# Kernel optimization log

Measured on AMD Instinct MI355X. Metric: run time of the kernel, lower is better.

The kernel has to match this reference:

```python
import jax, jax.numpy as jnp
import numpy as np

CLP_K = 9
SCL_KS = (3, 4, 3)  # scl0_k, scl1_k, scl2_k from the source


def _ste(f, x):
    # straight-through estimator: forward f(x), identity gradient
    return x + jax.lax.stop_gradient(f(x) - x)


def floor_ste(x):
    return _ste(jnp.floor, x)


def round_ste(x):
    return _ste(jnp.round, x)


def conv_t(x, w, b):
    # torch F.conv_transpose2d with kernel 5, stride 2, padding 2, output_padding 1
    # expressed as an lhs-dilated conv; w is torch layout [in, out, kh, kw]
    k = w.shape[-1]
    wc = jnp.flip(w, axis=(-2, -1)).transpose(1, 0, 2, 3)  # -> [out, in, kh, kw]
    lo = k - 1 - 2           # k-1-padding = 2
    hi = k - 1 - 2 + 1       # + output_padding = 3
    y = jax.lax.conv_general_dilated(
        x, wc, window_strides=(1, 1), padding=[(lo, hi), (lo, hi)],
        lhs_dilation=(2, 2), dimension_numbers=('NCHW', 'OIHW', 'NCHW'))
    return y + b[None, :, None, None]


def split_deconv(x, w, b, split):
    # sum of `split` transposed convs with floor((round(W)+j)/split) quantized weights
    out = 0.0
    for j in range(split):
        wj = floor_ste((round_ste(w) + j) / split)
        bj = floor_ste((round_ste(b) + j) / split)
        out = out + conv_t(x, wj, bj)
    return out


def _g_s_forward(x, ws, bs, ms, relus, dv, Bits, split):
    # clp[i] = round((2^Bits - 1) / relus[i] * 2^(16+clp_k))
    clp = jnp.round((2.0 ** Bits - 1.0) / relus * 2.0 ** (16 + CLP_K))
    for i in range(3):
        x = split_deconv(x, ws[i], bs[i], split)
        x = x * ms[i][None, :, None, None]
        x = floor_ste((x + 2.0 ** (dv[i] - 1 - CLP_K)) / 2.0 ** (dv[i] - CLP_K))
        x = jnp.clip(x, 0.0, clp[i])
        sk = SCL_KS[i]
        scl = floor_ste((relus[i] + 2.0 ** (sk - 1)) / 2.0 ** sk)
        x = floor_ste((x * scl + 2.0 ** (15 + CLP_K - sk)) / 2.0 ** (16 + CLP_K - sk))
    x = split_deconv(x, ws[3], bs[3], split)
    x = x * ms[3][None, :, None, None]
    x = floor_ste((x + 2.0 ** (dv[3] - 9)) / 2.0 ** (dv[3] - 8))
    return x / 255.0


def setup_inputs() -> dict:
    key = jax.random.key(0)
    ks = jax.random.split(key, 16)
    N, M = 192, 320
    B, h, w = 1, 48, 48
    x = jax.random.randint(ks[0], (B, M, h, w), 0, 256).astype(jnp.float32)
    w1 = jax.random.normal(ks[1], (M, N, 5, 5), jnp.float32) * 20.0
    b1 = jax.random.normal(ks[2], (N,), jnp.float32) * 20.0
    w2 = jax.random.normal(ks[3], (N, N, 5, 5), jnp.float32) * 20.0
    b2 = jax.random.normal(ks[4], (N,), jnp.float32) * 20.0
    w3 = jax.random.normal(ks[5], (N, N, 5, 5), jnp.float32) * 20.0
    b3 = jax.random.normal(ks[6], (N,), jnp.float32) * 20.0
    w4 = jax.random.normal(ks[7], (N, 3, 5, 5), jnp.float32) * 20.0
    b4 = jax.random.normal(ks[8], (3,), jnp.float32) * 20.0
    muls0 = jax.random.randint(ks[9], (N,), 1, 1000).astype(jnp.float32)
    muls1 = jax.random.randint(ks[10], (N,), 1, 1000).astype(jnp.float32)
    muls2 = jax.random.randint(ks[11], (N,), 1, 1000).astype(jnp.float32)
    muls3 = jax.random.randint(ks[12], (3,), 1, 1000).astype(jnp.float32)
    relus = jnp.array([40000.0, 36000.0, 30000.0], jnp.float32)
    muls_dvds = jnp.array([24, 24, 24, 24], jnp.int32)
    return {"x": x, "w1": w1, "b1": b1, "w2": w2, "b2": b2, "w3": w3,
            "b3": b3, "w4": w4, "b4": b4, "muls0": muls0, "muls1": muls1,
            "muls2": muls2, "muls3": muls3, "relus": relus,
            "muls_dvds": muls_dvds, "Bits": 8, "split": 4}


def reference(x, w1, b1, w2, b2, w3, b3, w4, b4,
              muls0, muls1, muls2, muls3, relus, muls_dvds, Bits, split):
    dv = muls_dvds.astype(jnp.float32)
    ws = (w1, w2, w3, w4)
    bs = (b1, b2, b3, b4)
    ms = (muls0, muls1, muls2, muls3)
    return _g_s_forward(x, ws, bs, ms, relus, dv, int(Bits), int(split))
```

## Files before the change

kernel.cpp:

```cpp
#include <hip/hip_runtime.h>
#include <cmath>


typedef int int4v  __attribute__((ext_vector_type(4)));
typedef int int16v __attribute__((ext_vector_type(16)));

__device__ __forceinline__ void tap_to_k(int t, int& ky, int& kx) {
    if (t < 9)       { int dy = t/3,  dx = t%3;                   ky = 4-2*dy; kx = 4-2*dx; }
    else if (t < 15) { int u = t-9;   int dy = u/2, dx = 1+(u&1);  ky = 4-2*dy; kx = 5-2*dx; }
    else if (t < 21) { int u = t-15;  int dy = 1+u/3, dx = u%3;    ky = 5-2*dy; kx = 4-2*dx; }
    else             { int u = t-21;  int dy = 1+u/2, dx = 1+(u&1); ky = 5-2*dy; kx = 5-2*dx; }
}

__global__ __launch_bounds__(256)
void convert_x_t(const float* __restrict__ x, signed char* __restrict__ xh,
                 int C, int HW) {
    __shared__ float t[64][65];
    const int p0 = blockIdx.x * 64;
    const int c0 = blockIdx.y * 64;
    const int pL = threadIdx.x & 63;
    const int r0 = threadIdx.x >> 6;
    #pragma unroll
    for (int k = 0; k < 16; ++k) {
        int ciL = r0 * 16 + k;
        t[ciL][pL] = x[(size_t)(c0 + ciL) * HW + p0 + pL];
    }
    __syncthreads();
    #pragma unroll
    for (int k = 0; k < 16; ++k) {
        int pL2 = r0 * 16 + k;
        xh[(size_t)(p0 + pL2) * C + c0 + pL] = (signed char)((int)t[pL][pL2] - 128);
    }
}

__global__ __launch_bounds__(256)
void pack3(const float* __restrict__ w1, const float* __restrict__ w2,
           const float* __restrict__ w3,
           signed char* __restrict__ p1, signed char* __restrict__ p2,
           signed char* __restrict__ p3) {
    const int layer = blockIdx.y;
    const float* w = (layer == 0) ? w1 : (layer == 1) ? w2 : w3;
    signed char* out = (layer == 0) ? p1 : (layer == 1) ? p2 : p3;
    const int Cin = (layer == 0) ? 320 : 192;
    const int Cout = 192, NT = 6;
    int idx = blockIdx.x * 256 + threadIdx.x;
    if (idx >= Cin * Cout) return;
    const int co = idx % Cout, ci = idx / Cout;
    const float* wr = w + (size_t)(ci * Cout + co) * 25;
    float v[25];
    #pragma unroll
    for (int k = 0; k < 25; ++k) {
        float t = rintf(wr[k]);
        v[k] = fminf(fmaxf(t, -128.0f), 127.0f);
    }
    const int qs = ci >> 5, half = (ci >> 4) & 1, j = ci & 15;
    const int nb = co >> 5, lane = half * 32 + (co & 31);
    size_t base = ((size_t)(qs * NT + nb) * 25) * 1024 + lane * 16 + j;
    #pragma unroll
    for (int t = 0; t < 25; ++t) {
        int ky, kx; tap_to_k(t, ky, kx);
        out[base + (size_t)t * 1024] = (signed char)(int)v[ky * 5 + kx];
    }
}

__global__ void pack_w4_i8(const float* __restrict__ w, signed char* __restrict__ wpk) {
    int idx = blockIdx.x * blockDim.x + threadIdx.x;
    if (idx >= 6 * 9 * 64 * 16) return;
    int j    = idx & 15;
    int lane = (idx >> 4) & 63;
    int rem  = idx >> 10;
    int s9   = rem % 9;
    int qs   = rem / 9;
    int col  = lane & 31;
    int co   = col & 7;
    int p    = col >> 3;
    int py = p >> 1, px = p & 1;
    int dy = s9 / 3, dx = s9 % 3;
    int ci = qs * 32 + ((lane >> 5) << 4) + j;
    bool part = (py == 0 || dy >= 1) && (px == 0 || dx >= 1);
    float v = 0.0f;
    if (co < 3 && part) {
        int ky = py ? 5 - 2 * dy : 4 - 2 * dy;
        int kx = px ? 5 - 2 * dx : 4 - 2 * dx;
        v = rintf(w[(size_t)(ci * 3 + co) * 25 + ky * 5 + kx]);
        v = fminf(fmaxf(v, -128.0f), 127.0f);
    }
    wpk[idx] = (signed char)(int)v;
}

__global__ __launch_bounds__(64)
void tap4(const float* __restrict__ w1, const float* __restrict__ w2,
          const float* __restrict__ w3, const float* __restrict__ w4,
          int* __restrict__ t1, int* __restrict__ t2,
          int* __restrict__ t3, int* __restrict__ t4) {
    const int layer = blockIdx.y;
    const float* w = (layer == 0) ? w1 : (layer == 1) ? w2 : (layer == 2) ? w3 : w4;
    int* ts = (layer == 0) ? t1 : (layer == 1) ? t2 : (layer == 2) ? t3 : t4;
    const int Cin = (layer == 0) ? 320 : 192;
    const int Cout = (layer == 3) ? 3 : 192;
    const int i = blockIdx.x;
    if (i >= 4 * Cout) return;
    const int co = i % Cout, p = i / Cout;
    const int py = p >> 1, px = p & 1;
    const int nky = (5 - py + 1) >> 1;
    const int nkx = (5 - px + 1) >> 1;
    const int ntap = nky * nkx;
    int s = 0;
    for (int idx = threadIdx.x; idx < Cin * ntap; idx += 64) {
        const int ci = idx / ntap;
        const int u  = idx - ci * ntap;
        const int ky = py + 2 * (u / nkx);
        const int kx = px + 2 * (u % nkx);
        float v = rintf(w[(size_t)(ci * Cout + co) * 25 + ky * 5 + kx]);
        v = fminf(fmaxf(v, -128.0f), 127.0f);
        s += (int)v;
    }
    #pragma unroll
    for (int off = 32; off > 0; off >>= 1)
        s += __shfl_down(s, off, 64);
    if (threadIdx.x == 0) ts[i] = s;
}

__device__ __forceinline__ constexpr int role_nt(int role, int s9) {
    constexpr int NT0[9] = {1,1,1,1,2,2,1,2,2};
    constexpr int NT1[9] = {0,1,1,1,2,2,1,2,2};
    return role == 0 ? NT0[s9] : NT1[s9];
}
__device__ __forceinline__ constexpr int role_tap(int role, int s9, int u) {
    constexpr int T0[9][2] = {{0,0},{1,0},{2,0},{3,0},{4,21},{5,22},{6,0},{7,23},{8,24}};
    constexpr int T1[9][2] = {{0,0},{9,0},{10,0},{15,0},{11,16},{12,17},{18,0},{13,19},{14,20}};
    return role == 0 ? T0[s9][u] : T1[s9][u];
}
__device__ __forceinline__ constexpr int role_acc(int role, int s9, int u) {
    constexpr int A0[9][2] = {{0,0},{0,0},{0,0},{0,0},{0,1},{0,1},{0,0},{0,1},{0,1}};
    constexpr int A1[9][2] = {{0,0},{0,0},{0,0},{1,0},{0,1},{0,1},{1,0},{0,1},{0,1}};
    return role == 0 ? A0[s9][u] : A1[s9][u];
}

template<int ROLE, int R>
__device__ __forceinline__ void compute_role(const signed char* xs, const signed char* bs,
                                             int16v (&acc)[R][2], const int (&p0)[R],
                                             int half, int lane) {
    #pragma unroll
    for (int s9 = 0; s9 < 9; ++s9) {
        if (role_nt(ROLE, s9) == 0) continue;
        const int dy = s9 / 3, dx = s9 % 3;
        int4v a[R];
        #pragma unroll
        for (int r = 0; r < R; ++r)
            a[r] = *(const int4v*)&xs[(p0[r] + dy * 18 + dx) * 48 + half * 16];
        #pragma unroll
        for (int u = 0; u < 2; ++u) {
            if (u < role_nt(ROLE, s9)) {
                int4v b = *(const int4v*)&bs[role_tap(ROLE, s9, u) * 1024 + lane * 16];
                const int ai = role_acc(ROLE, s9, u);
                #pragma unroll
                for (int r = 0; r < R; ++r)
                    acc[r][ai] = __builtin_amdgcn_mfma_i32_32x32x32_i8(a[r], b, acc[r][ai], 0, 0, 0);
            }
        }
    }
}

template<int MW>
__global__ __launch_bounds__(MW * 64, 3)
void deconv_v7(const signed char* __restrict__ xin, const signed char* __restrict__ wpk,
               const float* __restrict__ bias, const float* __restrict__ muls,
               const int* __restrict__ tsum,
               const float* __restrict__ relus, const int* __restrict__ dvds,
               const int* __restrict__ bitsp,
               int layer, int Cin, int Cout, int NT, int Hq, int Wq,
               signed char* __restrict__ outp) {
    constexpr int R = 2;
    constexpr int PAIRS = MW / 2;
    constexpr int NROW = PAIRS * R * 2 + 2;
    constexpr int NPIX = NROW * 18;
    constexpr int THREADS = MW * 64;
    constexpr int XC = NPIX * 2;
    constexpr int XI = (XC + THREADS - 1) / THREADS;
    constexpr int BC = 1600;
    constexpr int BI = (BC + THREADS - 1) / THREADS;

    __shared__ __align__(16) signed char xs[NPIX * 48];
    __shared__ __align__(16) signed char bs[25600];

    const int tid  = threadIdx.x;
    const int lane = tid & 63;
    const int wid  = tid >> 6;
    const int pairId = wid >> 1;
    const int role   = wid & 1;
    const int qx0  = blockIdx.y * 16;
    const int qy0  = blockIdx.z * (PAIRS * R * 2);
    const int nb   = blockIdx.x;
    const int n0   = nb * 32;

    int16v acc[R][2];
    #pragma unroll
    for (int r = 0; r < R; ++r)
        #pragma unroll
        for (int p = 0; p < 2; ++p)
            #pragma unroll
            for (int e = 0; e < 16; ++e) acc[r][p][e] = 0;

    const int half   = lane >> 5;
    const int rowbit = (lane >> 4) & 1;
    const int col    = lane & 15;
    int p0[R];
    #pragma unroll
    for (int r = 0; r < R; ++r)
        p0[r] = ((pairId * R + r) * 2 + rowbit) * 18 + col;

    int4v xreg[XI], breg[BI];

    auto load_chunk = [&](int ck) {
        const signed char* wslab = wpk + (size_t)((ck >> 5) * NT + nb) * 25600;
        #pragma unroll
        for (int t = 0; t < XI; ++t) {
            int i = tid + t * THREADS;
            if (i < XC) {
                int pix = i >> 1, g = i & 1;
                int rr = pix / 18, cc = pix - rr * 18;
                int y = qy0 - 1 + rr, xx = qx0 - 1 + cc;
                int4v v = {(int)0x80808080, (int)0x80808080,
                           (int)0x80808080, (int)0x80808080};
                if ((unsigned)y < (unsigned)Hq && (unsigned)xx < (unsigned)Wq)
                    v = *(const int4v*)&xin[((size_t)y * Wq + xx) * Cin + ck + g * 16];
                xreg[t] = v;
            }
        }
        #pragma unroll
        for (int t = 0; t < BI; ++t) {
            int i = tid + t * THREADS;
            if (i < BC) breg[t] = *(const int4v*)&wslab[(size_t)i * 16];
        }
    };
    auto store_chunk = [&]() {
        #pragma unroll
        for (int t = 0; t < XI; ++t) {
            int i = tid + t * THREADS;
            if (i < XC) {
                int pix = i >> 1, g = i & 1;
                *(int4v*)&xs[pix * 48 + g * 16] = xreg[t];
            }
        }
        #pragma unroll
        for (int t = 0; t < BI; ++t) {
            int i = tid + t * THREADS;
            if (i < BC) *(int4v*)&bs[i * 16] = breg[t];
        }
    };

    load_chunk(0);
    for (int ck = 0; ck < Cin; ck += 32) {
        __syncthreads();
        store_chunk();
        __syncthreads();
        if (ck + 32 < Cin) load_chunk(ck + 32);

        if (role == 0) compute_role<0, R>(xs, bs, acc, p0, half, lane);
        else           compute_role<1, R>(xs, bs, acc, p0, half, lane);
    }

    const int dv = dvds[layer];
    float add1 = ldexpf(1.0f, dv - 10);
    float inv1 = ldexpf(1.0f, -(dv - 9));
    const float relu = relus[layer];
    const int sk = (layer == 1) ? 4 : 3;
    const float bitsv = ldexpf(1.0f, bitsp[0]) - 1.0f;
    float clp, scl;
    {
        #pragma clang fp contract(off)
        clp = rintf(bitsv / relu * 33554432.0f);
        scl = floorf((relu + ldexpf(1.0f, sk - 1)) * ldexpf(1.0f, -sk));
    }
    float add2 = ldexpf(1.0f, 24 - sk);
    float inv2 = ldexpf(1.0f, -(25 - sk));

    const int co = n0 + (lane & 31);
    float bq = rintf(bias[co]);
    float mm = muls[co];
    int pmap[2];
    pmap[0] = role == 0 ? 0 : 1;
    pmap[1] = role == 0 ? 3 : 2;
    int fullp[2];
    #pragma unroll
    for (int a = 0; a < 2; ++a) fullp[a] = tsum[pmap[a] * Cout + co];

    const int Wout = Wq * 2;

    #pragma unroll
    for (int r = 0; r < R; ++r) {
        #pragma unroll
        for (int a = 0; a < 2; ++a) {
            const int p = pmap[a];
            const int py = p >> 1, px = p & 1;
            #pragma unroll
            for (int reg = 0; reg < 16; ++reg) {
                const int mrow = (reg & 3) + 8 * (reg >> 2) + 4 * (lane >> 5);
                const int qy = qy0 + (pairId * R + r) * 2 + (mrow >> 4);
                const int qx = qx0 + (mrow & 15);
                float v = (float)(acc[r][a][reg] + 128 * fullp[a]);
                {
                    #pragma clang fp contract(off)
                    v = (v + bq) * mm;
                    v = floorf((v + add1) * inv1);
                    v = fminf(fmaxf(v, 0.0f), clp);
                    v = floorf((v * scl + add2) * inv2);
                }
                const int oy = 2 * qy + py, ox = 2 * qx + px;
                outp[((size_t)oy * Wout + ox) * Cout + co] = (signed char)((int)v - 128);
            }
        }
    }
}

__global__ __launch_bounds__(512, 3)
void deconv_final_v7(const signed char* __restrict__ xin, const signed char* __restrict__ wpk,
                     const float* __restrict__ bias, const float* __restrict__ muls,
                     const int* __restrict__ tsum, const int* __restrict__ dvds,
                     int Cin, int Hq, int Wq, float* __restrict__ outp) {
    constexpr int R = 2, MW = 8;
    constexpr int NROW = MW * R * 2 + 2;
    constexpr int NPIX = NROW * 18;
    constexpr int THREADS = 512;
    constexpr int XC = NPIX * 2;
    constexpr int XI = (XC + THREADS - 1) / THREADS;
    constexpr int BC = 576;
    constexpr int BI = (BC + THREADS - 1) / THREADS;

    __shared__ __align__(16) signed char xs[NPIX * 48];
    __shared__ __align__(16) signed char bs[9216];

    const int tid  = threadIdx.x;
    const int lane = tid & 63;
    const int wid  = tid >> 6;
    const int qx0  = blockIdx.y * 16;
    const int qy0  = blockIdx.z * (MW * R * 2);

    int16v acc[R];
    #pragma unroll
    for (int r = 0; r < R; ++r)
        #pragma unroll
        for (int e = 0; e < 16; ++e) acc[r][e] = 0;

    const int half   = lane >> 5;
    const int rowbit = (lane >> 4) & 1;
    const int col    = lane & 15;
    int p0[R];
    #pragma unroll
    for (int r = 0; r < R; ++r)
        p0[r] = ((wid * R + r) * 2 + rowbit) * 18 + col;

    int4v xreg[XI], breg[BI];

    auto load_chunk = [&](int ck) {
        const signed char* wslab = wpk + (size_t)(ck >> 5) * 9216;
        #pragma unroll
        for (int t = 0; t < XI; ++t) {
            int i = tid + t * THREADS;
            if (i < XC) {
                int pix = i >> 1, g = i & 1;
                int rr = pix / 18, cc = pix - rr * 18;
                int y = qy0 - 1 + rr, xx = qx0 - 1 + cc;
                int4v v = {(int)0x80808080, (int)0x80808080,
                           (int)0x80808080, (int)0x80808080};
                if ((unsigned)y < (unsigned)Hq && (unsigned)xx < (unsigned)Wq)
                    v = *(const int4v*)&xin[((size_t)y * Wq + xx) * Cin + ck + g * 16];
                xreg[t] = v;
            }
        }
        #pragma unroll
        for (int t = 0; t < BI; ++t) {
            int i = tid + t * THREADS;
            if (i < BC) breg[t] = *(const int4v*)&wslab[(size_t)i * 16];
        }
    };
    auto store_chunk = [&]() {
        #pragma unroll
        for (int t = 0; t < XI; ++t) {
            int i = tid + t * THREADS;
            if (i < XC) {
                int pix = i >> 1, g = i & 1;
                *(int4v*)&xs[pix * 48 + g * 16] = xreg[t];
            }
        }
        #pragma unroll
        for (int t = 0; t < BI; ++t) {
            int i = tid + t * THREADS;
            if (i < BC) *(int4v*)&bs[i * 16] = breg[t];
        }
    };

    load_chunk(0);
    for (int ck = 0; ck < Cin; ck += 32) {
        __syncthreads();
        store_chunk();
        __syncthreads();
        if (ck + 32 < Cin) load_chunk(ck + 32);

        #pragma unroll
        for (int s9 = 0; s9 < 9; ++s9) {
            const int dy = s9 / 3, dx = s9 % 3;
            int4v b = *(const int4v*)&bs[s9 * 1024 + lane * 16];
            #pragma unroll
            for (int r = 0; r < R; ++r) {
                int4v a = *(const int4v*)&xs[(p0[r] + dy * 18 + dx) * 48 + half * 16];
                acc[r] = __builtin_amdgcn_mfma_i32_32x32x32_i8(a, b, acc[r], 0, 0, 0);
            }
        }
    }

    const int dv = dvds[3];
    const float add1 = ldexpf(1.0f, dv - 9);
    const float inv1 = ldexpf(1.0f, -(dv - 8));

    const int coln = lane & 31;
    const int co = coln & 7;
    const int p  = coln >> 3;
    const int py = p >> 1, px = p & 1;
    const bool valid = (co < 3);
    float bq = 0.f, mm = 0.f;
    int fp = 0;
    if (valid) { bq = rintf(bias[co]); mm = muls[co]; fp = tsum[p * 3 + co]; }

    const int Wout = Wq * 2, Hout = Hq * 2;
    #pragma unroll
    for (int r = 0; r < R; ++r) {
        #pragma unroll
        for (int reg = 0; reg < 16; ++reg) {
            const int mrow = (reg & 3) + 8 * (reg >> 2) + 4 * (lane >> 5);
            const int qy = qy0 + (wid * R + r) * 2 + (mrow >> 4);
            const int qx = qx0 + (mrow & 15);
            float v = (float)(acc[r][reg] + 128 * fp);
            {
                #pragma clang fp contract(off)
                v = (v + bq) * mm;
                v = floorf((v + add1) * inv1);
                v = v / 255.0f;
            }
            if (valid) {
                const int oy = 2 * qy + py, ox = 2 * qx + px;
                outp[((size_t)co * Hout + oy) * Wout + ox] = v;
            }
        }
    }
}

extern "C" void kernel_launch(void* const* d_in, const int* in_sizes, int n_in,
                              void* d_out, int out_size, void* d_ws, size_t ws_size,
                              hipStream_t stream) {
    const float* x  = (const float*)d_in[0];
    const float* w1 = (const float*)d_in[1];
    const float* b1 = (const float*)d_in[2];
    const float* w2 = (const float*)d_in[3];
    const float* b2 = (const float*)d_in[4];
    const float* w3 = (const float*)d_in[5];
    const float* b3 = (const float*)d_in[6];
    const float* w4 = (const float*)d_in[7];
    const float* b4 = (const float*)d_in[8];
    const float* m0 = (const float*)d_in[9];
    const float* m1 = (const float*)d_in[10];
    const float* m2 = (const float*)d_in[11];
    const float* m3 = (const float*)d_in[12];
    const float* relus = (const float*)d_in[13];
    const int* dvds = (const int*)d_in[14];
    const int* bitsp = (const int*)d_in[15];

    signed char* wsb = (signed char*)d_ws;
    size_t o = 0;
    signed char* wpk1 = wsb + o; o += (size_t)10 * 6 * 25600;
    signed char* wpk2 = wsb + o; o += (size_t)6 * 6 * 25600;
    signed char* wpk3 = wsb + o; o += (size_t)6 * 6 * 25600;
    signed char* wpk4 = wsb + o; o += (size_t)6 * 9216;
    int* ts1 = (int*)(wsb + o); o += 4 * 192 * 4;
    int* ts2 = (int*)(wsb + o); o += 4 * 192 * 4;
    int* ts3 = (int*)(wsb + o); o += 4 * 192 * 4;
    int* ts4 = (int*)(wsb + o); o += 4 * 4 * 4;
    o = (o + 15) & ~(size_t)15;
    signed char* xh = wsb + o; o += (size_t)48 * 48 * 320;
    signed char* a1 = wsb + o; o += (size_t)96 * 96 * 192;
    signed char* a2 = wsb + o; o += (size_t)192 * 192 * 192;
    signed char* a3 = wsb + o; o += (size_t)384 * 384 * 192;

    convert_x_t<<<dim3(36, 5), 256, 0, stream>>>(x, xh, 320, 48 * 48);
    pack3<<<dim3(240, 3), 256, 0, stream>>>(w1, w2, w3, wpk1, wpk2, wpk3);
    pack_w4_i8<<<(6 * 9 * 1024 + 255) / 256, 256, 0, stream>>>(w4, wpk4);
    tap4<<<dim3(768, 4), 64, 0, stream>>>(w1, w2, w3, w4, ts1, ts2, ts3, ts4);

    deconv_v7<4><<<dim3(6, 3, 6), 256, 0, stream>>>(
        xh, wpk1, b1, m0, ts1, relus, dvds, bitsp, 0, 320, 192, 6, 48, 48, a1);
    deconv_v7<8><<<dim3(6, 6, 6), 512, 0, stream>>>(
        a1, wpk2, b2, m1, ts2, relus, dvds, bitsp, 1, 192, 192, 6, 96, 96, a2);
    deconv_v7<8><<<dim3(6, 12, 12), 512, 0, stream>>>(
        a2, wpk3, b3, m2, ts3, relus, dvds, bitsp, 2, 192, 192, 6, 192, 192, a3);
    deconv_final_v7<<<dim3(1, 24, 12), 512, 0, stream>>>(
        a3, wpk4, b4, m3, ts4, dvds, 192, 384, 384, (float*)d_out);
}
```

Before: 224.4 us.

## Fuse tap-sum computation into weight packing and raise occupancy bounds

```diff
diff --git a/kernel.cpp b/kernel.cpp
--- a/kernel.cpp
+++ b/kernel.cpp
@@ -14,7 +14,9 @@
 
 __global__ __launch_bounds__(256)
 void convert_x_t(const float* __restrict__ x, signed char* __restrict__ xh,
-                 int C, int HW) {
+                 int* __restrict__ tsz, int ts_count, int C, int HW) {
+    if (blockIdx.x == 0 && blockIdx.y == 0)
+        for (int i = threadIdx.x; i < ts_count; i += 256) tsz[i] = 0;
     __shared__ float t[64][65];
     const int p0 = blockIdx.x * 64;
     const int c0 = blockIdx.y * 64;
@@ -34,32 +36,56 @@
 }
 
 __global__ __launch_bounds__(256)
-void pack3(const float* __restrict__ w1, const float* __restrict__ w2,
+void packA(const float* __restrict__ w1, const float* __restrict__ w2,
            const float* __restrict__ w3,
            signed char* __restrict__ p1, signed char* __restrict__ p2,
-           signed char* __restrict__ p3) {
+           signed char* __restrict__ p3,
+           int* __restrict__ t1, int* __restrict__ t2, int* __restrict__ t3) {
     const int layer = blockIdx.y;
     const float* w = (layer == 0) ? w1 : (layer == 1) ? w2 : w3;
     signed char* out = (layer == 0) ? p1 : (layer == 1) ? p2 : p3;
-    const int Cin = (layer == 0) ? 320 : 192;
-    const int Cout = 192, NT = 6;
-    int idx = blockIdx.x * 256 + threadIdx.x;
-    if (idx >= Cin * Cout) return;
-    const int co = idx % Cout, ci = idx / Cout;
-    const float* wr = w + (size_t)(ci * Cout + co) * 25;
-    float v[25];
-    #pragma unroll
-    for (int k = 0; k < 25; ++k) {
-        float t = rintf(wr[k]);
-        v[k] = fminf(fmaxf(t, -128.0f), 127.0f);
-    }
-    const int qs = ci >> 5, half = (ci >> 4) & 1, j = ci & 15;
-    const int nb = co >> 5, lane = half * 32 + (co & 31);
-    size_t base = ((size_t)(qs * NT + nb) * 25) * 1024 + lane * 16 + j;
-    #pragma unroll
-    for (int t = 0; t < 25; ++t) {
-        int ky, kx; tap_to_k(t, ky, kx);
-        out[base + (size_t)t * 1024] = (signed char)(int)v[ky * 5 + kx];
+    int* ts = (layer == 0) ? t1 : (layer == 1) ? t2 : t3;
+    const int Cout = 192;
+    const int s = blockIdx.x;
+    if (layer > 0 && s >= 36) return;
+    const int qs = s / 6, nb = s % 6;
+
+    __shared__ __align__(16) signed char ls[25600];
+    __shared__ int lsum[4][32];
+    if (threadIdx.x < 128) ((int*)lsum)[threadIdx.x] = 0;
+    __syncthreads();
+
+    #pragma unroll
+    for (int k = 0; k < 4; ++k) {
+        const int pidx = threadIdx.x + k * 256;
+        const int cil = pidx >> 5;
+        const int col = pidx & 31;
+        const int ci = qs * 32 + cil;
+        const int co = nb * 32 + col;
+        const float* wr = w + (size_t)(ci * Cout + co) * 25;
+        const int half = cil >> 4, j = cil & 15;
+        const int base = (half * 32 + col) * 16 + j;
+        int psum[4] = {0, 0, 0, 0};
+        #pragma unroll
+        for (int t = 0; t < 25; ++t) {
+            int ky, kx; tap_to_k(t, ky, kx);
+            float v = rintf(wr[ky * 5 + kx]);
+            v = fminf(fmaxf(v, -128.0f), 127.0f);
+            int iv = (int)v;
+            ls[t * 1024 + base] = (signed char)iv;
+            psum[((ky & 1) << 1) | (kx & 1)] += iv;
+        }
+        #pragma unroll
+        for (int p = 0; p < 4; ++p) atomicAdd(&lsum[p][col], psum[p]);
+    }
+    __syncthreads();
+
+    signed char* dst = out + (size_t)s * 25600;
+    for (int i = threadIdx.x; i < 1600; i += 256)
+        *(int4v*)&dst[i * 16] = *(const int4v*)&ls[i * 16];
+    if (threadIdx.x < 128) {
+        const int p = threadIdx.x >> 5, col = threadIdx.x & 31;
+        atomicAdd(&ts[p * Cout + nb * 32 + col], lsum[p][col]);
     }
 }
 
@@ -89,17 +115,9 @@
 }
 
 __global__ __launch_bounds__(64)
-void tap4(const float* __restrict__ w1, const float* __restrict__ w2,
-          const float* __restrict__ w3, const float* __restrict__ w4,
-          int* __restrict__ t1, int* __restrict__ t2,
-          int* __restrict__ t3, int* __restrict__ t4) {
-    const int layer = blockIdx.y;
-    const float* w = (layer == 0) ? w1 : (layer == 1) ? w2 : (layer == 2) ? w3 : w4;
-    int* ts = (layer == 0) ? t1 : (layer == 1) ? t2 : (layer == 2) ? t3 : t4;
-    const int Cin = (layer == 0) ? 320 : 192;
-    const int Cout = (layer == 3) ? 3 : 192;
+void tap_w4(const float* __restrict__ w, int* __restrict__ ts) {
+    const int Cin = 192, Cout = 3;
     const int i = blockIdx.x;
-    if (i >= 4 * Cout) return;
     const int co = i % Cout, p = i / Cout;
     const int py = p >> 1, px = p & 1;
     const int nky = (5 - py + 1) >> 1;
@@ -163,8 +181,8 @@
 }
 
 template<int MW>
-__global__ __launch_bounds__(MW * 64, 3)
-void deconv_v7(const signed char* __restrict__ xin, const signed char* __restrict__ wpk,
+__global__ __launch_bounds__(MW * 64, MW == 8 ? 4 : 3)
+void deconv_v8(const signed char* __restrict__ xin, const signed char* __restrict__ wpk,
                const float* __restrict__ bias, const float* __restrict__ muls,
                const int* __restrict__ tsum,
                const float* __restrict__ relus, const int* __restrict__ dvds,
@@ -314,8 +332,8 @@
     }
 }
 
-__global__ __launch_bounds__(512, 3)
-void deconv_final_v7(const signed char* __restrict__ xin, const signed char* __restrict__ wpk,
+__global__ __launch_bounds__(512, 4)
+void deconv_final_v8(const signed char* __restrict__ xin, const signed char* __restrict__ wpk,
                      const float* __restrict__ bias, const float* __restrict__ muls,
                      const int* __restrict__ tsum, const int* __restrict__ dvds,
                      int Cin, int Hq, int Wq, float* __restrict__ outp) {
@@ -482,17 +500,19 @@
     signed char* a2 = wsb + o; o += (size_t)192 * 192 * 192;
     signed char* a3 = wsb + o; o += (size_t)384 * 384 * 192;
 
-    convert_x_t<<<dim3(36, 5), 256, 0, stream>>>(x, xh, 320, 48 * 48);
-    pack3<<<dim3(240, 3), 256, 0, stream>>>(w1, w2, w3, wpk1, wpk2, wpk3);
+    const int ts_count = 4 * 192 * 3 + 4 * 4;
+
+    convert_x_t<<<dim3(36, 5), 256, 0, stream>>>(x, xh, ts1, ts_count, 320, 48 * 48);
+    packA<<<dim3(60, 3), 256, 0, stream>>>(w1, w2, w3, wpk1, wpk2, wpk3, ts1, ts2, ts3);
     pack_w4_i8<<<(6 * 9 * 1024 + 255) / 256, 256, 0, stream>>>(w4, wpk4);
-    tap4<<<dim3(768, 4), 64, 0, stream>>>(w1, w2, w3, w4, ts1, ts2, ts3, ts4);
-
-    deconv_v7<4><<<dim3(6, 3, 6), 256, 0, stream>>>(
+    tap_w4<<<12, 64, 0, stream>>>(w4, ts4);
+
+    deconv_v8<4><<<dim3(6, 3, 6), 256, 0, stream>>>(
         xh, wpk1, b1, m0, ts1, relus, dvds, bitsp, 0, 320, 192, 6, 48, 48, a1);
-    deconv_v7<8><<<dim3(6, 6, 6), 512, 0, stream>>>(
+    deconv_v8<8><<<dim3(6, 6, 6), 512, 0, stream>>>(
         a1, wpk2, b2, m1, ts2, relus, dvds, bitsp, 1, 192, 192, 6, 96, 96, a2);
-    deconv_v7<8><<<dim3(6, 12, 12), 512, 0, stream>>>(
+    deconv_v8<8><<<dim3(6, 12, 12), 512, 0, stream>>>(
         a2, wpk3, b3, m2, ts3, relus, dvds, bitsp, 2, 192, 192, 6, 192, 192, a3);
-    deconv_final_v7<<<dim3(1, 24, 12), 512, 0, stream>>>(
+    deconv_final_v8<<<dim3(1, 24, 12), 512, 0, stream>>>(
         a3, wpk4, b4, m3, ts4, dvds, 192, 384, 384, (float*)d_out);
 }
```

Result: faster. 211.5 us (-5.7%).
